# Kernel optimization log

Measured on AMD Instinct MI355X. Metric: run time of the kernel, lower is better.

Reference implementation:

```python
import jax, jax.numpy as jnp
import numpy as np
import math

D_MODEL = 1024
N_HEADS = 16
D_K = D_MODEL // N_HEADS
R_TYPES = 8
B, S = 2, 2048


def setup_inputs() -> dict:
    key = jax.random.key(0)
    ks = jax.random.split(key, 12)
    sc = 0.02
    return {
        "x": jax.random.normal(ks[0], (B, S, D_MODEL), jnp.float32),
        "Wq": jax.random.normal(ks[1], (D_MODEL, D_MODEL), jnp.float32) * sc,
        "bq": jax.random.normal(ks[2], (D_MODEL,), jnp.float32) * sc,
        "Wk": jax.random.normal(ks[3], (D_MODEL, D_MODEL), jnp.float32) * sc,
        "bk": jax.random.normal(ks[4], (D_MODEL,), jnp.float32) * sc,
        "Wv": jax.random.normal(ks[5], (D_MODEL, D_MODEL), jnp.float32) * sc,
        "bv": jax.random.normal(ks[6], (D_MODEL,), jnp.float32) * sc,
        "Wo": jax.random.normal(ks[7], (D_MODEL, D_MODEL), jnp.float32) * sc,
        "bo": jax.random.normal(ks[8], (D_MODEL,), jnp.float32) * sc,
        "resource_bias": jax.random.normal(ks[9], (N_HEADS, R_TYPES, R_TYPES), jnp.float32),
        "resource_mask": jax.random.randint(ks[10], (B, S), 0, R_TYPES, jnp.int32),
        "attention_mask": jnp.ones((B, S), jnp.int32),
    }


def reference(x, resource_mask, attention_mask, Wq, bq, Wk, bk, Wv, bv, Wo, bo, resource_bias):
    # torch nn.Linear: y = x @ W.T + b
    def lin(h, W, b):
        return jnp.einsum("bsd,ed->bse", h, W) + b

    def split_heads(t):  # [B,S,D] -> [B,H,S,d_k]
        return t.reshape(B, S, N_HEADS, D_K).transpose(0, 2, 1, 3)

    Q = split_heads(lin(x, Wq, bq))
    K = split_heads(lin(x, Wk, bk))
    V = split_heads(lin(x, Wv, bv))

    scores = jnp.einsum("bhid,bhjd->bhij", Q, K) / math.sqrt(D_K)  # [B,H,S,S]

    # vectorized resource-bias gather: bias[h, r_i, r_j] added to scores[b,h,i,j]
    r = resource_mask.astype(jnp.int32)  # values guaranteed < R_TYPES
    # resource_bias[:, r[b,i], r[b,j]] -> [B,H,S,S]
    bias = resource_bias[:, r[:, :, None], r[:, None, :]]  # [H,B,S,S]
    scores = scores + bias.transpose(1, 0, 2, 3)

    mask = attention_mask[:, None, None, :]  # [B,1,1,S] broadcast to [B,H,S,S]
    scores = jnp.where(mask == 0, jnp.float32(-1e9), scores)

    attn = jax.nn.softmax(scores, axis=-1)  # dropout is identity in eval
    out = jnp.einsum("bhij,bhjd->bhid", attn, V)
    out = out.transpose(0, 2, 1, 3).reshape(B, S, D_MODEL)
    return jnp.einsum("bsd,ed->bse", out, Wo) + bo
```

## Files before the change

### kernel.cpp

```cpp
#include <hip/hip_runtime.h>
#include <cstdint>

#define D_MODEL 1024
#define NHEADS  16
#define DKH     64
#define SEQ     2048
#define NBATCH  2
#define MROWS   (NBATCH*SEQ)
#define RTYPES  8
#define LOG2E   1.44269504f

typedef __bf16 bf16;
typedef __bf16 bf16x4v __attribute__((ext_vector_type(4)));
typedef __bf16 bf16x8v __attribute__((ext_vector_type(8)));
typedef float  f32x4v  __attribute__((ext_vector_type(4)));
typedef float  f32x16v __attribute__((ext_vector_type(16)));

typedef unsigned int __attribute__((address_space(1))) as1_u32;
typedef unsigned int __attribute__((address_space(3))) as3_u32;

static __device__ __forceinline__ void gload_lds16(const void* g, void* l) {
  __builtin_amdgcn_global_load_lds((const as1_u32*)(uintptr_t)g,
                                   (as3_u32*)(uintptr_t)l, 16, 0, 0);
}

static __device__ __forceinline__ f32x4v mfma16(bf16x8v a, bf16x8v b, f32x4v c) {
  return __builtin_amdgcn_mfma_f32_16x16x32_bf16(a, b, c, 0, 0, 0);
}
static __device__ __forceinline__ f32x16v mfma32(bf16x8v a, bf16x8v b, f32x16v c) {
  return __builtin_amdgcn_mfma_f32_32x32x16_bf16(a, b, c, 0, 0, 0);
}

__global__ void convert_kernel(const float* __restrict__ x,  const float* __restrict__ wq,
                               const float* __restrict__ wk, const float* __restrict__ wv,
                               const float* __restrict__ wo,
                               bf16* __restrict__ xb,  bf16* __restrict__ wqb,
                               bf16* __restrict__ wkb, bf16* __restrict__ wvb,
                               bf16* __restrict__ wob,
                               const float* __restrict__ rbias,
                               const int* __restrict__ rmask,
                               const int* __restrict__ amask,
                               float* __restrict__ biasg)
{
  int idx = blockIdx.x*256 + threadIdx.x;
  if (idx < 1048576){
    float4 v = ((const float4*)x)[idx];
    bf16x4v o = { (bf16)v.x, (bf16)v.y, (bf16)v.z, (bf16)v.w };
    ((bf16x4v*)xb)[idx] = o;
  } else if (idx < 2097152){
    int r = (idx - 1048576) >> 18;
    int i = (idx - 1048576) & 262143;
    const float* src; bf16* dst;
    if (r == 0)      { src = wq; dst = wqb; }
    else if (r == 1) { src = wk; dst = wkb; }
    else if (r == 2) { src = wv; dst = wvb; }
    else             { src = wo; dst = wob; }
    float4 v = ((const float4*)src)[i];
    bf16x4v o = { (bf16)v.x, (bf16)v.y, (bf16)v.z, (bf16)v.w };
    ((bf16x4v*)dst)[i] = o;
  } else {
    int i = idx - 2097152;
    #pragma unroll
    for (int bb=0; bb<NBATCH; bb++){
      int id2 = bb*(NHEADS*RTYPES*SEQ) + i;
      int j  = id2 & (SEQ-1);
      int t  = (id2 >> 11) & 7;
      int hh = (id2 >> 14) & 15;
      int rj = rmask[bb*SEQ + j];
      float am = amask[bb*SEQ + j] ? 0.f : -1e9f;
      biasg[id2] = (rbias[(hh*RTYPES + t)*RTYPES + rj] + am) * LOG2E;
    }
  }
}

struct GemmOuts { const bf16* W[3]; const float* bia[3]; void* out[3]; };

template<int FUSED>
__global__ __launch_bounds__(256, 3) void gemm_bt_kernel(
    const bf16* __restrict__ A, GemmOuts args, float qscale)
{
  const int K  = D_MODEL;
  const int z  = FUSED ? blockIdx.z : 0;
  const bf16*  Bw   = args.W[z];
  const float* bias = args.bia[z];
  void* outp        = args.out[z];
  const float scale = (FUSED && z==0) ? qscale : 1.0f;

  const int n0 = blockIdx.x*128, m0 = blockIdx.y*128;
  const int tid = threadIdx.x;
  const int w = tid>>6, lane = tid&63, g = lane>>4, c = lane&15;
  const int wm = w>>1, wn = w&1;

  __shared__ __align__(16) bf16 a_lds[2][128*32];
  __shared__ __align__(16) bf16 b_lds[2][128*32];

  const f32x4v fzero = {0.f,0.f,0.f,0.f};
  f32x4v acc[4][4];
  for (int i=0;i<4;i++) for (int j=0;j<4;j++) acc[i][j] = fzero;

  const int srow = tid>>2, sc8 = tid&3;

  auto STAGE = [&](int k0, int nb){
    gload_lds16(A  + (size_t)(m0+srow)*K     + k0 + sc8*8, &a_lds[nb][(w*64)*8]);
    gload_lds16(Bw + (size_t)(n0+srow)*K     + k0 + sc8*8, &b_lds[nb][(w*64)*8]);
    gload_lds16(A  + (size_t)(m0+64+srow)*K  + k0 + sc8*8, &a_lds[nb][(256 + w*64)*8]);
    gload_lds16(Bw + (size_t)(n0+64+srow)*K  + k0 + sc8*8, &b_lds[nb][(256 + w*64)*8]);
  };

  auto COMPUTE = [&](int nb){
    bf16x8v af[4], bfv[4];
    #pragma unroll
    for (int mt=0;mt<4;mt++)
      af[mt] = *(const bf16x8v*)&a_lds[nb][(wm*64 + mt*16 + c)*32 + g*8];
    #pragma unroll
    for (int nt=0;nt<4;nt++)
      bfv[nt] = *(const bf16x8v*)&b_lds[nb][(wn*64 + nt*16 + c)*32 + g*8];
    #pragma unroll
    for (int mt=0;mt<4;mt++)
      #pragma unroll
      for (int nt=0;nt<4;nt++)
        acc[mt][nt] = mfma16(af[mt], bfv[nt], acc[mt][nt]);
  };

  STAGE(0, 0);
  __syncthreads();
  int cur = 0;
  for (int k0=32; k0<K; k0+=32){
    STAGE(k0, cur^1);
    COMPUTE(cur);
    __syncthreads();
    cur ^= 1;
  }
  COMPUTE(cur);

  #pragma unroll
  for (int mt=0;mt<4;mt++){
    #pragma unroll
    for (int nt=0;nt<4;nt++){
      if (FUSED && z == 2){
        int m = m0 + wm*64 + mt*16 + g*4;
        int n = n0 + wn*64 + nt*16 + c;
        int bb=m>>11, s=m&2047, hh=n>>6, dk=n&63;
        float bn = bias[n];
        bf16x4v ov;
        #pragma unroll
        for (int r=0;r<4;r++) ov[r] = (bf16)(acc[mt][nt][r] + bn);
        *(bf16x4v*)&((bf16*)outp)[(((size_t)bb*NHEADS+hh)*DKH + dk)*SEQ + s] = ov;
      } else {
        #pragma unroll
        for (int r=0;r<4;r++){
          int m = m0 + wm*64 + mt*16 + g*4 + r;
          int n = n0 + wn*64 + nt*16 + c;
          float v = acc[mt][nt][r] + bias[n];
          if (FUSED){
            v *= scale;
            int bb=m>>11, s=m&2047, hh=n>>6, dk=n&63;
            ((bf16*)outp)[(((size_t)bb*NHEADS+hh)*SEQ + s)*DKH + dk] = (bf16)v;
          } else {
            ((float*)outp)[(size_t)m*D_MODEL + n] = v;
          }
        }
      }
    }
  }
}

__global__ __launch_bounds__(512, 4) void attn7_kernel(
    const bf16* __restrict__ Qg, const bf16* __restrict__ Kg,
    const bf16* __restrict__ Vtg, const float* __restrict__ biasg,
    const int* __restrict__ rmask, bf16* __restrict__ Og)
{
  const int b = blockIdx.z, h = blockIdx.y, q0 = blockIdx.x*128;
  const int tid = threadIdx.x;
  const int w = tid>>6, lane = tid&63;
  const int half = w>>2, wl = w&3;
  const int q5 = lane&31, hi = lane>>5;
  const int bh = b*NHEADS + h;
  const int NTl = 16;

  __shared__ __align__(16) bf16  kv_lds[2][2][2][4096];
  __shared__ __align__(16) float bias_lds[2][2][512];

  const int qrow = q0 + wl*32 + q5;
  const bf16* qptr = Qg + ((size_t)bh*SEQ + qrow)*DKH;
  bf16x8v qf[4];
  #pragma unroll
  for (int kc=0;kc<4;kc++)
    qf[kc] = *(const bf16x8v*)(qptr + kc*16 + hi*8);

  const int tq = rmask[b*SEQ + qrow];

  int boff[2][4];
  #pragma unroll
  for (int nt=0;nt<2;nt++){
    const int j00 = nt*32 + hi*8;
    boff[nt][0] = tq*64 + ((j00 +  0) ^ (tq*8));
    boff[nt][1] = tq*64 + ((j00 +  4) ^ (tq*8));
    boff[nt][2] = tq*64 + ((j00 + 16) ^ (tq*8));
    boff[nt][3] = tq*64 + ((j00 + 20) ^ (tq*8));
  }

  f32x16v oacc0, oacc1;
  #pragma unroll
  for (int r=0;r<16;r++){ oacc0[r]=0.f; oacc1[r]=0.f; }
  float mrow = -1e30f, lrow = 0.f;

  const int sig = (lane & 0x33) | ((lane & 8) >> 1) | ((lane & 4) << 1);
  const bf16* ksrcL = Kg  + ((size_t)bh*SEQ + sig)*DKH;
  const bf16* vsrcL = Vtg + ((size_t)bh*DKH + lane)*SEQ;
  const int jb0 = half*1024;
  const int lbase = hi*512 + q5*8;

  auto STAGE = [&](int t, int nb){
    const int j0 = jb0 + t*64;
    #pragma unroll
    for (int i=0;i<2;i++){
      const int dblk = i*4 + wl;
      gload_lds16(ksrcL + (size_t)j0*DKH + dblk*8, &kv_lds[half][nb][0][dblk*512]);
      gload_lds16(vsrcL + j0 + dblk*8,             &kv_lds[half][nb][1][dblk*512]);
    }
    if (wl < 2){
      const int chunk = wl*64 + lane;
      const int tcls = chunk>>4, c16 = chunk&15;
      const int jsw = (c16<<2) ^ (tcls<<3);
      gload_lds16(biasg + ((size_t)(bh*RTYPES + tcls))*SEQ + j0 + jsw,
                  &bias_lds[half][nb][wl*256]);
    }
  };

  auto COMPUTE = [&](int nb){
    const bf16*  kb_ = &kv_lds[half][nb][0][0];
    const bf16*  vb_ = &kv_lds[half][nb][1][0];
    const float* bb_ = &bias_lds[half][nb][0];

    f32x16v s0, s1;
    #pragma unroll
    for (int g4=0; g4<4; g4++){
      f32x4v b0 = *(const f32x4v*)&bb_[boff[0][g4]];
      f32x4v b1 = *(const f32x4v*)&bb_[boff[1][g4]];
      #pragma unroll
      for (int rr=0; rr<4; rr++){ s0[g4*4+rr] = b0[rr]; s1[g4*4+rr] = b1[rr]; }
    }

    #pragma unroll
    for (int kc=0;kc<4;kc++){
      bf16x8v kf0 = *(const bf16x8v*)(kb_ + lbase + kc*1024);
      bf16x8v kf1 = *(const bf16x8v*)(kb_ + lbase + kc*1024 + 256);
      s0 = mfma32(kf0, qf[kc], s0);
      s1 = mfma32(kf1, qf[kc], s1);
    }

    float a0 = fmaxf(fmaxf(s0[0],s0[1]),s0[2]);
    float a1 = fmaxf(fmaxf(s0[3],s0[4]),s0[5]);
    float a2 = fmaxf(fmaxf(s0[6],s0[7]),s0[8]);
    float a3 = fmaxf(fmaxf(s0[9],s0[10]),s0[11]);
    float a4 = fmaxf(fmaxf(s0[12],s0[13]),s0[14]);
    float a5 = fmaxf(fmaxf(s0[15],s1[0]),s1[1]);
    float a6 = fmaxf(fmaxf(s1[2],s1[3]),s1[4]);
    float a7 = fmaxf(fmaxf(s1[5],s1[6]),s1[7]);
    float a8 = fmaxf(fmaxf(s1[8],s1[9]),s1[10]);
    float a9 = fmaxf(fmaxf(s1[11],s1[12]),s1[13]);
    float aA = fmaxf(s1[14],s1[15]);
    float b0 = fmaxf(fmaxf(a0,a1),a2);
    float b1 = fmaxf(fmaxf(a3,a4),a5);
    float b2 = fmaxf(fmaxf(a6,a7),a8);
    float b3 = fmaxf(a9,aA);
    float mx = fmaxf(fmaxf(b0,b1), fmaxf(b2,b3));
    mx = fmaxf(mx, __shfl_xor(mx, 32));

    if (!__all(mx - mrow <= 8.0f)){
      float mnew = fmaxf(mrow, mx);
      float scl = exp2f(mrow - mnew);
      #pragma unroll
      for (int r=0;r<16;r++){ oacc0[r] *= scl; oacc1[r] *= scl; }
      lrow *= scl;
      mrow = mnew;
    }

    #pragma unroll
    for (int r=0;r<16;r++){ s0[r] = exp2f(s0[r] - mrow); s1[r] = exp2f(s1[r] - mrow); }

    float t0 = 0.f, t1 = 0.f;
    #pragma unroll
    for (int r=0;r<16;r++){ t0 += s0[r]; t1 += s1[r]; }
    float sum = t0 + t1;
    sum += __shfl_xor(sum, 32);
    lrow += sum;

    bf16x8v pa0, pa1, pa2, pa3;
    #pragma unroll
    for (int e=0;e<8;e++){
      pa0[e] = (bf16)s0[e];   pa1[e] = (bf16)s0[e+8];
      pa2[e] = (bf16)s1[e];   pa3[e] = (bf16)s1[e+8];
    }

    #pragma unroll
    for (int m=0;m<4;m++){
      bf16x8v vf0 = *(const bf16x8v*)(vb_ + lbase + m*1024);
      bf16x8v vf1 = *(const bf16x8v*)(vb_ + lbase + m*1024 + 256);
      bf16x8v pm = (m==0)?pa0:(m==1)?pa1:(m==2)?pa2:pa3;
      oacc0 = mfma32(vf0, pm, oacc0);
      oacc1 = mfma32(vf1, pm, oacc1);
    }
  };

  STAGE(0, 0);
  __syncthreads();
  int cur = 0;
  #pragma unroll 1
  for (int t=0; t<NTl; ++t){
    if (t+1 < NTl) STAGE(t+1, cur^1);
    COMPUTE(cur);
    __syncthreads();
    cur ^= 1;
  }

  float* mrg = (float*)&kv_lds[0][0][0][0];
  if (half == 1){
    float* row = mrg + (wl*32 + q5)*68;
    #pragma unroll
    for (int rq=0;rq<4;rq++){
      f32x4v t0v, t1v;
      #pragma unroll
      for (int k=0;k<4;k++){ t0v[k] = oacc0[rq*4+k]; t1v[k] = oacc1[rq*4+k]; }
      *(f32x4v*)(row + 0  + rq*8 + hi*4) = t0v;
      *(f32x4v*)(row + 32 + rq*8 + hi*4) = t1v;
    }
    if (hi == 0){ row[64] = mrow; row[65] = lrow; }
  }
  __syncthreads();
  if (half == 0){
    const float* row = mrg + (wl*32 + q5)*68;
    const float m1 = row[64], l1 = row[65];
    const float M  = fmaxf(mrow, m1);
    const float s0c = exp2f(mrow - M), s1c = exp2f(m1 - M);
    const float inv = 1.0f / (lrow*s0c + l1*s1c);
    bf16* orow = &Og[(size_t)(b*SEQ + qrow)*D_MODEL + h*DKH];
    #pragma unroll
    for (int rq=0;rq<4;rq++){
      f32x4v o1a = *(const f32x4v*)(row + 0  + rq*8 + hi*4);
      f32x4v o1b = *(const f32x4v*)(row + 32 + rq*8 + hi*4);
      bf16x4v ov0, ov1;
      #pragma unroll
      for (int k=0;k<4;k++){
        ov0[k] = (bf16)((oacc0[rq*4+k]*s0c + o1a[k]*s1c) * inv);
        ov1[k] = (bf16)((oacc1[rq*4+k]*s0c + o1b[k]*s1c) * inv);
      }
      const int d = 8*rq + 4*hi;
      *(bf16x4v*)(orow + d)      = ov0;
      *(bf16x4v*)(orow + 32 + d) = ov1;
    }
  }
}

extern "C" void kernel_launch(void* const* d_in, const int* in_sizes, int n_in,
                              void* d_out, int out_size, void* d_ws, size_t ws_size,
                              hipStream_t stream)
{
  (void)in_sizes; (void)n_in; (void)out_size; (void)ws_size;
  const float* x     = (const float*)d_in[0];
  const float* Wq    = (const float*)d_in[1];
  const float* bq    = (const float*)d_in[2];
  const float* Wk    = (const float*)d_in[3];
  const float* bk    = (const float*)d_in[4];
  const float* Wv    = (const float*)d_in[5];
  const float* bv    = (const float*)d_in[6];
  const float* Wo    = (const float*)d_in[7];
  const float* bo    = (const float*)d_in[8];
  const float* rbias = (const float*)d_in[9];
  const int*   rmask = (const int*)d_in[10];
  const int*   amask = (const int*)d_in[11];
  float* out = (float*)d_out;

  char* ws = (char*)d_ws;
  bf16*  xb    = (bf16*)(ws);
  bf16*  wqb   = (bf16*)(ws + (8u<<20));
  bf16*  wkb   = (bf16*)(ws + (10u<<20));
  bf16*  wvb   = (bf16*)(ws + (12u<<20));
  bf16*  wob   = (bf16*)(ws + (14u<<20));
  bf16*  qb    = (bf16*)(ws + (16u<<20));
  bf16*  kb    = (bf16*)(ws + (24u<<20));
  bf16*  vtb   = (bf16*)(ws + (32u<<20));
  bf16*  aob   = (bf16*)(ws + (40u<<20));
  float* biasg = (float*)(ws + (48u<<20));

  convert_kernel<<<9216, 256, 0, stream>>>(x,Wq,Wk,Wv,Wo, xb,wqb,wkb,wvb,wob,
                                           rbias, rmask, amask, biasg);

  GemmOuts qkv;
  qkv.W[0]=wqb; qkv.W[1]=wkb; qkv.W[2]=wvb;
  qkv.bia[0]=bq; qkv.bia[1]=bk; qkv.bia[2]=bv;
  qkv.out[0]=qb; qkv.out[1]=kb; qkv.out[2]=vtb;
  gemm_bt_kernel<1><<<dim3(D_MODEL/128, MROWS/128, 3), 256, 0, stream>>>(xb, qkv, 0.125f*LOG2E);

  attn7_kernel<<<dim3(SEQ/128, NHEADS, NBATCH), 512, 0, stream>>>(qb, kb, vtb, biasg, rmask, aob);

  GemmOuts og;
  og.W[0]=wob; og.W[1]=wob; og.W[2]=wob;
  og.bia[0]=bo; og.bia[1]=bo; og.bia[2]=bo;
  og.out[0]=out; og.out[1]=out; og.out[2]=out;
  gemm_bt_kernel<0><<<dim3(D_MODEL/128, MROWS/128), 256, 0, stream>>>(aob, og, 1.0f);
}
```

Before: 134.5 us.

## Compute softmax row sums with MFMA and pre-swizzle bias table layout

The per-tile row-sum reduction (32 scalar adds plus a cross-lane shuffle) is replaced by four MFMA ops that multiply a ones vector by the probability fragments, accumulating into an extra 16-register accumulator. Separately, the bias table is now written by the convert kernel in the exact per-tile swizzled order the attention kernel consumes, so the LDS staging load becomes a contiguous copy with simpler addressing. The cost is extra matrix-core work and register pressure from the additional accumulator, which could hurt occupancy at the given launch bounds.

Result: slower. 150.7 us (+12.1%).

```diff
diff --git a/kernel.cpp b/kernel.cpp
--- a/kernel.cpp
+++ b/kernel.cpp
@@ -60,15 +60,18 @@
     ((bf16x4v*)dst)[i] = o;
   } else {
     int i = idx - 2097152;
+    int W    = i & 63;
+    int t    = (i>>6) & 7;
+    int tile = (i>>9) & 31;
+    int hh   = i >> 14;
+    int X  = W ^ (t*4);
+    int nt = X >> 5, h2 = (X>>4)&1, r = X & 15;
+    int j  = tile*64 + nt*32 + h2*8 + (r&7) + 16*(r>>3);
     #pragma unroll
     for (int bb=0; bb<NBATCH; bb++){
-      int id2 = bb*(NHEADS*RTYPES*SEQ) + i;
-      int j  = id2 & (SEQ-1);
-      int t  = (id2 >> 11) & 7;
-      int hh = (id2 >> 14) & 15;
       int rj = rmask[bb*SEQ + j];
       float am = amask[bb*SEQ + j] ? 0.f : -1e9f;
-      biasg[id2] = (rbias[(hh*RTYPES + t)*RTYPES + rj] + am) * LOG2E;
+      biasg[bb*262144 + i] = (rbias[(hh*RTYPES + t)*RTYPES + rj] + am) * LOG2E;
     }
   }
 }
@@ -165,7 +168,7 @@
   }
 }
 
-__global__ __launch_bounds__(512, 4) void attn7_kernel(
+__global__ __launch_bounds__(512, 4) void attn8_kernel(
     const bf16* __restrict__ Qg, const bf16* __restrict__ Kg,
     const bf16* __restrict__ Vtg, const float* __restrict__ biasg,
     const int* __restrict__ rmask, bf16* __restrict__ Og)
@@ -192,22 +195,24 @@
 
   int boff[2][4];
   #pragma unroll
-  for (int nt=0;nt<2;nt++){
-    const int j00 = nt*32 + hi*8;
-    boff[nt][0] = tq*64 + ((j00 +  0) ^ (tq*8));
-    boff[nt][1] = tq*64 + ((j00 +  4) ^ (tq*8));
-    boff[nt][2] = tq*64 + ((j00 + 16) ^ (tq*8));
-    boff[nt][3] = tq*64 + ((j00 + 20) ^ (tq*8));
-  }
-
-  f32x16v oacc0, oacc1;
+  for (int nt=0;nt<2;nt++)
+    #pragma unroll
+    for (int k=0;k<4;k++)
+      boff[nt][k] = tq*64 + ((nt*32 + hi*16 + k*4) ^ (tq*4));
+
+  bf16x8v ones;
   #pragma unroll
-  for (int r=0;r<16;r++){ oacc0[r]=0.f; oacc1[r]=0.f; }
-  float mrow = -1e30f, lrow = 0.f;
+  for (int i=0;i<8;i++) ones[i] = (bf16)1.0f;
+
+  f32x16v oacc0, oacc1, lacc;
+  #pragma unroll
+  for (int r=0;r<16;r++){ oacc0[r]=0.f; oacc1[r]=0.f; lacc[r]=0.f; }
+  float mrow = -1e30f;
 
   const int sig = (lane & 0x33) | ((lane & 8) >> 1) | ((lane & 4) << 1);
-  const bf16* ksrcL = Kg  + ((size_t)bh*SEQ + sig)*DKH;
-  const bf16* vsrcL = Vtg + ((size_t)bh*DKH + lane)*SEQ;
+  const bf16*  ksrcL = Kg  + ((size_t)bh*SEQ + sig)*DKH;
+  const bf16*  vsrcL = Vtg + ((size_t)bh*DKH + lane)*SEQ;
+  const float* biasB = biasg + (size_t)b*262144 + h*16384;
   const int jb0 = half*1024;
   const int lbase = hi*512 + q5*8;
 
@@ -221,9 +226,7 @@
     }
     if (wl < 2){
       const int chunk = wl*64 + lane;
-      const int tcls = chunk>>4, c16 = chunk&15;
-      const int jsw = (c16<<2) ^ (tcls<<3);
-      gload_lds16(biasg + ((size_t)(bh*RTYPES + tcls))*SEQ + j0 + jsw,
+      gload_lds16(biasB + (size_t)(half*16 + t)*512 + chunk*4,
                   &bias_lds[half][nb][wl*256]);
     }
   };
@@ -235,11 +238,11 @@
 
     f32x16v s0, s1;
     #pragma unroll
-    for (int g4=0; g4<4; g4++){
-      f32x4v b0 = *(const f32x4v*)&bb_[boff[0][g4]];
-      f32x4v b1 = *(const f32x4v*)&bb_[boff[1][g4]];
+    for (int k=0;k<4;k++){
+      f32x4v b0 = *(const f32x4v*)&bb_[boff[0][k]];
+      f32x4v b1 = *(const f32x4v*)&bb_[boff[1][k]];
       #pragma unroll
-      for (int rr=0; rr<4; rr++){ s0[g4*4+rr] = b0[rr]; s1[g4*4+rr] = b1[rr]; }
+      for (int e=0;e<4;e++){ s0[k*4+e] = b0[e]; s1[k*4+e] = b1[e]; }
     }
 
     #pragma unroll
@@ -272,20 +275,12 @@
       float mnew = fmaxf(mrow, mx);
       float scl = exp2f(mrow - mnew);
       #pragma unroll
-      for (int r=0;r<16;r++){ oacc0[r] *= scl; oacc1[r] *= scl; }
-      lrow *= scl;
+      for (int r=0;r<16;r++){ oacc0[r] *= scl; oacc1[r] *= scl; lacc[r] *= scl; }
       mrow = mnew;
     }
 
     #pragma unroll
     for (int r=0;r<16;r++){ s0[r] = exp2f(s0[r] - mrow); s1[r] = exp2f(s1[r] - mrow); }
-
-    float t0 = 0.f, t1 = 0.f;
-    #pragma unroll
-    for (int r=0;r<16;r++){ t0 += s0[r]; t1 += s1[r]; }
-    float sum = t0 + t1;
-    sum += __shfl_xor(sum, 32);
-    lrow += sum;
 
     bf16x8v pa0, pa1, pa2, pa3;
     #pragma unroll
@@ -293,6 +288,11 @@
       pa0[e] = (bf16)s0[e];   pa1[e] = (bf16)s0[e+8];
       pa2[e] = (bf16)s1[e];   pa3[e] = (bf16)s1[e+8];
     }
+
+    lacc = mfma32(ones, pa0, lacc);
+    lacc = mfma32(ones, pa1, lacc);
+    lacc = mfma32(ones, pa2, lacc);
+    lacc = mfma32(ones, pa3, lacc);
 
     #pragma unroll
     for (int m=0;m<4;m++){
@@ -326,7 +326,7 @@
       *(f32x4v*)(row + 0  + rq*8 + hi*4) = t0v;
       *(f32x4v*)(row + 32 + rq*8 + hi*4) = t1v;
     }
-    if (hi == 0){ row[64] = mrow; row[65] = lrow; }
+    if (hi == 0){ row[64] = mrow; row[65] = lacc[0]; }
   }
   __syncthreads();
   if (half == 0){
@@ -334,7 +334,7 @@
     const float m1 = row[64], l1 = row[65];
     const float M  = fmaxf(mrow, m1);
     const float s0c = exp2f(mrow - M), s1c = exp2f(m1 - M);
-    const float inv = 1.0f / (lrow*s0c + l1*s1c);
+    const float inv = 1.0f / (lacc[0]*s0c + l1*s1c);
     bf16* orow = &Og[(size_t)(b*SEQ + qrow)*D_MODEL + h*DKH];
     #pragma unroll
     for (int rq=0;rq<4;rq++){
@@ -393,7 +393,7 @@
   qkv.out[0]=qb; qkv.out[1]=kb; qkv.out[2]=vtb;
   gemm_bt_kernel<1><<<dim3(D_MODEL/128, MROWS/128, 3), 256, 0, stream>>>(xb, qkv, 0.125f*LOG2E);
 
-  attn7_kernel<<<dim3(SEQ/128, NHEADS, NBATCH), 512, 0, stream>>>(qb, kb, vtb, biasg, rmask, aob);
+  attn8_kernel<<<dim3(SEQ/128, NHEADS, NBATCH), 512, 0, stream>>>(qb, kb, vtb, biasg, rmask, aob);
 
   GemmOuts og;
   og.W[0]=wob; og.W[1]=wob; og.W[2]=wob;
```

## Fold resource bias and attention mask into extra QK head dimensions

Applied to the files above, without the earlier changes.

Extends Q and K rows from 64 to 80 columns. Q carries the per-row bias table entries for its resource type plus a large negative mask coefficient, and K carries a one-hot resource type plus a mask indicator, so the QK MFMA computes scores+bias+mask directly. This removes the precomputed float bias tensor, its LDS staging, and the per-tile bias loads and initialisation. In exchange it adds one more MFMA k-chunk per tile and more K load traffic, and the bias is now held in bf16 precision.

Result: no change. 134.3 us (-0.1%).

```diff
diff --git a/kernel.cpp b/kernel.cpp
--- a/kernel.cpp
+++ b/kernel.cpp
@@ -4,6 +4,7 @@
 #define D_MODEL 1024
 #define NHEADS  16
 #define DKH     64
+#define DEXT    80
 #define SEQ     2048
 #define NBATCH  2
 #define MROWS   (NBATCH*SEQ)
@@ -40,7 +41,7 @@
                                const float* __restrict__ rbias,
                                const int* __restrict__ rmask,
                                const int* __restrict__ amask,
-                               float* __restrict__ biasg)
+                               bf16* __restrict__ qext, bf16* __restrict__ kext)
 {
   int idx = blockIdx.x*256 + threadIdx.x;
   if (idx < 1048576){
@@ -60,16 +61,30 @@
     ((bf16x4v*)dst)[i] = o;
   } else {
     int i = idx - 2097152;
-    #pragma unroll
-    for (int bb=0; bb<NBATCH; bb++){
-      int id2 = bb*(NHEADS*RTYPES*SEQ) + i;
-      int j  = id2 & (SEQ-1);
-      int t  = (id2 >> 11) & 7;
-      int hh = (id2 >> 14) & 15;
-      int rj = rmask[bb*SEQ + j];
-      float am = amask[bb*SEQ + j] ? 0.f : -1e9f;
-      biasg[id2] = (rbias[(hh*RTYPES + t)*RTYPES + rj] + am) * LOG2E;
-    }
+    int s  = i & 2047;
+    int hh = (i>>11) & 15;
+    int bb = (i>>15) & 1;
+    int which = i >> 16;
+    int t  = rmask[bb*SEQ + s];
+    int am = amask[bb*SEQ + s];
+    bf16* dst = (which==0 ? qext : kext)
+              + ((size_t)(bb*NHEADS + hh)*SEQ + s)*DEXT + 64;
+    bf16x8v lo, hi2;
+    if (which == 0){
+      #pragma unroll
+      for (int r=0;r<8;r++) lo[r] = (bf16)(rbias[(hh*RTYPES + t)*RTYPES + r] * LOG2E);
+      #pragma unroll
+      for (int r=0;r<8;r++) hi2[r] = (bf16)0.f;
+      hi2[0] = (bf16)(-1048576.0f);
+    } else {
+      #pragma unroll
+      for (int r=0;r<8;r++) lo[r] = (bf16)((t==r) ? 1.f : 0.f);
+      #pragma unroll
+      for (int r=0;r<8;r++) hi2[r] = (bf16)0.f;
+      hi2[0] = am ? (bf16)0.f : (bf16)1.0f;
+    }
+    *(bf16x8v*)dst       = lo;
+    *(bf16x8v*)(dst + 8) = hi2;
   }
 }
 
@@ -155,7 +170,7 @@
           if (FUSED){
             v *= scale;
             int bb=m>>11, s=m&2047, hh=n>>6, dk=n&63;
-            ((bf16*)outp)[(((size_t)bb*NHEADS+hh)*SEQ + s)*DKH + dk] = (bf16)v;
+            ((bf16*)outp)[(((size_t)bb*NHEADS+hh)*SEQ + s)*DEXT + dk] = (bf16)v;
           } else {
             ((float*)outp)[(size_t)m*D_MODEL + n] = v;
           }
@@ -165,10 +180,9 @@
   }
 }
 
-__global__ __launch_bounds__(512, 4) void attn7_kernel(
+__global__ __launch_bounds__(512, 4) void attn9_kernel(
     const bf16* __restrict__ Qg, const bf16* __restrict__ Kg,
-    const bf16* __restrict__ Vtg, const float* __restrict__ biasg,
-    const int* __restrict__ rmask, bf16* __restrict__ Og)
+    const bf16* __restrict__ Vtg, bf16* __restrict__ Og)
 {
   const int b = blockIdx.z, h = blockIdx.y, q0 = blockIdx.x*128;
   const int tid = threadIdx.x;
@@ -178,27 +192,15 @@
   const int bh = b*NHEADS + h;
   const int NTl = 16;
 
-  __shared__ __align__(16) bf16  kv_lds[2][2][2][4096];
-  __shared__ __align__(16) float bias_lds[2][2][512];
+  __shared__ __align__(16) bf16 k_lds[2][2][5120];
+  __shared__ __align__(16) bf16 v_lds[2][2][4096];
 
   const int qrow = q0 + wl*32 + q5;
-  const bf16* qptr = Qg + ((size_t)bh*SEQ + qrow)*DKH;
-  bf16x8v qf[4];
+  const bf16* qptr = Qg + ((size_t)bh*SEQ + qrow)*DEXT;
+  bf16x8v qf[5];
   #pragma unroll
-  for (int kc=0;kc<4;kc++)
+  for (int kc=0;kc<5;kc++)
     qf[kc] = *(const bf16x8v*)(qptr + kc*16 + hi*8);
-
-  const int tq = rmask[b*SEQ + qrow];
-
-  int boff[2][4];
-  #pragma unroll
-  for (int nt=0;nt<2;nt++){
-    const int j00 = nt*32 + hi*8;
-    boff[nt][0] = tq*64 + ((j00 +  0) ^ (tq*8));
-    boff[nt][1] = tq*64 + ((j00 +  4) ^ (tq*8));
-    boff[nt][2] = tq*64 + ((j00 + 16) ^ (tq*8));
-    boff[nt][3] = tq*64 + ((j00 + 20) ^ (tq*8));
-  }
 
   f32x16v oacc0, oacc1;
   #pragma unroll
@@ -206,44 +208,31 @@
   float mrow = -1e30f, lrow = 0.f;
 
   const int sig = (lane & 0x33) | ((lane & 8) >> 1) | ((lane & 4) << 1);
-  const bf16* ksrcL = Kg  + ((size_t)bh*SEQ + sig)*DKH;
+  const bf16* ksrcL = Kg  + ((size_t)bh*SEQ + sig)*DEXT;
   const bf16* vsrcL = Vtg + ((size_t)bh*DKH + lane)*SEQ;
   const int jb0 = half*1024;
   const int lbase = hi*512 + q5*8;
 
   auto STAGE = [&](int t, int nb){
     const int j0 = jb0 + t*64;
-    #pragma unroll
-    for (int i=0;i<2;i++){
-      const int dblk = i*4 + wl;
-      gload_lds16(ksrcL + (size_t)j0*DKH + dblk*8, &kv_lds[half][nb][0][dblk*512]);
-      gload_lds16(vsrcL + j0 + dblk*8,             &kv_lds[half][nb][1][dblk*512]);
-    }
-    if (wl < 2){
-      const int chunk = wl*64 + lane;
-      const int tcls = chunk>>4, c16 = chunk&15;
-      const int jsw = (c16<<2) ^ (tcls<<3);
-      gload_lds16(biasg + ((size_t)(bh*RTYPES + tcls))*SEQ + j0 + jsw,
-                  &bias_lds[half][nb][wl*256]);
-    }
+    const size_t joff = (size_t)j0*DEXT;
+    gload_lds16(ksrcL + joff + wl*8,       &k_lds[half][nb][wl*512]);
+    gload_lds16(ksrcL + joff + (wl+4)*8,   &k_lds[half][nb][(wl+4)*512]);
+    if (wl < 2)
+      gload_lds16(ksrcL + joff + (8+wl)*8, &k_lds[half][nb][(8+wl)*512]);
+    gload_lds16(vsrcL + j0 + wl*8,         &v_lds[half][nb][wl*512]);
+    gload_lds16(vsrcL + j0 + (wl+4)*8,     &v_lds[half][nb][(wl+4)*512]);
   };
 
   auto COMPUTE = [&](int nb){
-    const bf16*  kb_ = &kv_lds[half][nb][0][0];
-    const bf16*  vb_ = &kv_lds[half][nb][1][0];
-    const float* bb_ = &bias_lds[half][nb][0];
+    const bf16* kb_ = &k_lds[half][nb][0];
+    const bf16* vb_ = &v_lds[half][nb][0];
 
     f32x16v s0, s1;
     #pragma unroll
-    for (int g4=0; g4<4; g4++){
-      f32x4v b0 = *(const f32x4v*)&bb_[boff[0][g4]];
-      f32x4v b1 = *(const f32x4v*)&bb_[boff[1][g4]];
-      #pragma unroll
-      for (int rr=0; rr<4; rr++){ s0[g4*4+rr] = b0[rr]; s1[g4*4+rr] = b1[rr]; }
-    }
-
-    #pragma unroll
-    for (int kc=0;kc<4;kc++){
+    for (int r=0;r<16;r++){ s0[r]=0.f; s1[r]=0.f; }
+    #pragma unroll
+    for (int kc=0;kc<5;kc++){
       bf16x8v kf0 = *(const bf16x8v*)(kb_ + lbase + kc*1024);
       bf16x8v kf1 = *(const bf16x8v*)(kb_ + lbase + kc*1024 + 256);
       s0 = mfma32(kf0, qf[kc], s0);
@@ -315,7 +304,7 @@
     cur ^= 1;
   }
 
-  float* mrg = (float*)&kv_lds[0][0][0][0];
+  float* mrg = (float*)&k_lds[0][0][0];
   if (half == 1){
     float* row = mrg + (wl*32 + q5)*68;
     #pragma unroll
@@ -379,13 +368,12 @@
   bf16*  wvb   = (bf16*)(ws + (12u<<20));
   bf16*  wob   = (bf16*)(ws + (14u<<20));
   bf16*  qb    = (bf16*)(ws + (16u<<20));
-  bf16*  kb    = (bf16*)(ws + (24u<<20));
-  bf16*  vtb   = (bf16*)(ws + (32u<<20));
-  bf16*  aob   = (bf16*)(ws + (40u<<20));
-  float* biasg = (float*)(ws + (48u<<20));
-
-  convert_kernel<<<9216, 256, 0, stream>>>(x,Wq,Wk,Wv,Wo, xb,wqb,wkb,wvb,wob,
-                                           rbias, rmask, amask, biasg);
+  bf16*  kb    = (bf16*)(ws + (27u<<20));
+  bf16*  vtb   = (bf16*)(ws + (38u<<20));
+  bf16*  aob   = (bf16*)(ws + (46u<<20));
+
+  convert_kernel<<<8704, 256, 0, stream>>>(x,Wq,Wk,Wv,Wo, xb,wqb,wkb,wvb,wob,
+                                           rbias, rmask, amask, qb, kb);
 
   GemmOuts qkv;
   qkv.W[0]=wqb; qkv.W[1]=wkb; qkv.W[2]=wvb;
@@ -393,7 +381,7 @@
   qkv.out[0]=qb; qkv.out[1]=kb; qkv.out[2]=vtb;
   gemm_bt_kernel<1><<<dim3(D_MODEL/128, MROWS/128, 3), 256, 0, stream>>>(xb, qkv, 0.125f*LOG2E);
 
-  attn7_kernel<<<dim3(SEQ/128, NHEADS, NBATCH), 512, 0, stream>>>(qb, kb, vtb, biasg, rmask, aob);
+  attn9_kernel<<<dim3(SEQ/128, NHEADS, NBATCH), 512, 0, stream>>>(qb, kb, vtb, aob);
 
   GemmOuts og;
   og.W[0]=wob; og.W[1]=wob; og.W[2]=wob;
```
